# Kernel optimization log

Measured on AMD Instinct MI355X. Metric: run time of the kernel, lower is better.

## Reference

```python
import jax, jax.numpy as jnp
import numpy as np

B, S, D = 4, 4096, 1024
C = 8.0

def setup_inputs() -> dict:
    key = jax.random.key(0)
    k_x, k_wa, k_wx, k_ba, k_bx, k_lam = jax.random.split(key, 6)
    x = jax.random.normal(k_x, (B, S, D), dtype=jnp.float32)
    std = 1.0 / np.sqrt(D)
    Wa = jax.random.normal(k_wa, (D, D), dtype=jnp.float32) * std
    Wx = jax.random.normal(k_wx, (D, D), dtype=jnp.float32) * std
    ba = jax.random.normal(k_ba, (D,), dtype=jnp.float32) * 0.02
    bx = jax.random.normal(k_bx, (D,), dtype=jnp.float32) * 0.02
    # Lambda init: u ~ U(0.9, 0.999); Lambda = -log(u^{-1/c} - 1)
    u = jax.random.uniform(k_lam, (D,), dtype=jnp.float32, minval=0.9, maxval=0.999)
    Lam = -jnp.log(jnp.power(u, -1.0 / C) - 1.0)
    return {"x": x, "Wa": Wa, "Wx": Wx, "ba": ba, "bx": bx, "Lam": Lam}

def reference(x, Wa, Wx, ba, bx, Lam):
    # gates for all timesteps at once (two GEMMs)
    rt = jax.nn.sigmoid(jnp.einsum('bsd,hd->bsh', x, Wa) + ba)   # recurrence gate
    it = jax.nn.sigmoid(jnp.einsum('bsd,hd->bsh', x, Wx) + bx)   # input gate
    log_a = -C * jax.nn.softplus(-Lam) * rt                      # (B,S,D)
    a = jnp.exp(log_a)
    b = jnp.sqrt(1.0 - a * a) * (it * x)                         # (B,S,D)
    # sequential diagonal linear recurrence h_t = a_t * h_{t-1} + b_t
    def step(h, ab):
        a_t, b_t = ab
        h = a_t * h + b_t
        return h, h
    h0 = jnp.zeros((x.shape[0], x.shape[2]), dtype=x.dtype)
    _, y = jax.lax.scan(step, h0, (jnp.swapaxes(a, 0, 1), jnp.swapaxes(b, 0, 1)))
    return jnp.swapaxes(y, 0, 1)  # (B,S,D)
```

## Files before the change

### kernel.cpp

```cpp
#include <hip/hip_runtime.h>
#include <hip/hip_bf16.h>
#include <math.h>

#define BDIM 4
#define SLEN 4096
#define DDIM 1024
#define MROWS (BDIM*SLEN)
#define KDIM DDIM
#define NCHUNK 64
#define CLEN (SLEN/NCHUNK)
#define NCH (BDIM*DDIM)
#define NKT (KDIM/32)
#define LDSBUF 16384

typedef __bf16 bf16;
typedef __bf16 bf16x8 __attribute__((ext_vector_type(8)));
typedef float f32x16 __attribute__((ext_vector_type(16)));

__device__ __forceinline__ void gload_lds16(const void* g, void* l) {
  __builtin_amdgcn_global_load_lds(
      (const __attribute__((address_space(1))) unsigned int*)g,
      (__attribute__((address_space(3))) unsigned int*)l, 16, 0, 0);
}

__global__ void cast_swz_kernel(const float* __restrict__ in, bf16* __restrict__ out) {
  const int gid  = blockIdx.x * 256 + threadIdx.x;
  const int tile = gid >> 7, local = gid & 127;
  const int j = local & 3, r = local >> 2;
  const int T = tile >> 5, KT = tile & 31;
  const float4* src = (const float4*)(in + (size_t)(T*32 + r) * KDIM + KT*32 + j*8);
  float4 v0 = src[0], v1 = src[1];
  bf16x8 o;
  o[0] = (bf16)v0.x; o[1] = (bf16)v0.y; o[2] = (bf16)v0.z; o[3] = (bf16)v0.w;
  o[4] = (bf16)v1.x; o[5] = (bf16)v1.y; o[6] = (bf16)v1.z; o[7] = (bf16)v1.w;
  ((bf16x8*)out)[(size_t)tile * 128 + j*32 + r] = o;
}

__global__ void klam_kernel(const float* __restrict__ Lam, float* __restrict__ klam) {
  int h = blockIdx.x * blockDim.x + threadIdx.x;
  if (h < DDIM) klam[h] = -8.0f * log1pf(__expf(-Lam[h]));
}

__global__ __launch_bounds__(256, 3) void gemm_gates_kernel(
    const bf16* __restrict__ xb, const bf16* __restrict__ wab, const bf16* __restrict__ wxb,
    const float* __restrict__ ba, const float* __restrict__ bx,
    const float* __restrict__ klam, float* __restrict__ Aarr, bf16* __restrict__ Bp,
    float* __restrict__ sAo, float* __restrict__ sBo)
{
  __shared__ char smem[3*LDSBUF];

  const int tid  = threadIdx.x;
  const int wave = tid >> 6, lane = tid & 63;
  const int wm = wave >> 1, wn = wave & 1;

  const int orig  = blockIdx.x;
  const int newid = (orig & 7) * 256 + (orig >> 3);
  const int m0 = (newid >> 4) * 128;
  const int h0 = (newid & 15) * 64;

  f32x16 accA0 = (f32x16)0.0f, accA1 = (f32x16)0.0f;
  f32x16 accX0 = (f32x16)0.0f, accX1 = (f32x16)0.0f;

  const int Tb = m0 >> 5;
  const int Ht = h0 >> 5;
  const bf16* xsrc0 = xb  + (size_t)(Tb + (tid >> 7)) * 32768 + (tid & 127) * 8;
  const bf16* xsrc1 = xsrc0 + 2 * 32768;
  const bf16* wsrcA = wab + (size_t)(Ht + (tid >> 7)) * 32768 + (tid & 127) * 8;
  const bf16* wsrcX = wxb + (size_t)(Ht + (tid >> 7)) * 32768 + (tid & 127) * 8;

  auto STAGE = [&](int KT, char* nb) {
    gload_lds16(xsrc0 + KT*1024, nb + tid*16);
    gload_lds16(xsrc1 + KT*1024, nb + 4096  + tid*16);
    gload_lds16(wsrcA + KT*1024, nb + 8192  + tid*16);
    gload_lds16(wsrcX + KT*1024, nb + 12288 + tid*16);
  };

  const int awoff  = wm*4096  + lane*16;
  const int bwoffA = 8192  + wn*2048 + lane*16;
  const int bwoffX = 12288 + wn*2048 + lane*16;

  char* b0 = smem;
  char* b1 = smem + LDSBUF;
  char* b2 = smem + 2*LDSBUF;

  STAGE(0, b0);
  STAGE(1, b1);
  asm volatile("s_waitcnt vmcnt(4)" ::: "memory");
  __builtin_amdgcn_s_barrier();

  char *pc = b0, *pn = b1, *ps = b2;
  for (int kt = 0; kt < NKT; ++kt) {
    bf16x8 a00 = *(const bf16x8*)(pc + awoff);
    bf16x8 a01 = *(const bf16x8*)(pc + awoff + 1024);
    bf16x8 a10 = *(const bf16x8*)(pc + awoff + 2048);
    bf16x8 a11 = *(const bf16x8*)(pc + awoff + 3072);
    bf16x8 ba0 = *(const bf16x8*)(pc + bwoffA);
    bf16x8 ba1 = *(const bf16x8*)(pc + bwoffA + 1024);
    bf16x8 bx0 = *(const bf16x8*)(pc + bwoffX);
    bf16x8 bx1 = *(const bf16x8*)(pc + bwoffX + 1024);
    __builtin_amdgcn_sched_barrier(0);

    if (kt + 2 < NKT) STAGE(kt + 2, ps);

    __builtin_amdgcn_s_barrier();
    asm volatile("s_waitcnt lgkmcnt(0)" ::: "memory");
    __builtin_amdgcn_sched_barrier(0);

    __builtin_amdgcn_s_setprio(1);
    accA0 = __builtin_amdgcn_mfma_f32_32x32x16_bf16(a00, ba0, accA0, 0, 0, 0);
    accA1 = __builtin_amdgcn_mfma_f32_32x32x16_bf16(a10, ba0, accA1, 0, 0, 0);
    accX0 = __builtin_amdgcn_mfma_f32_32x32x16_bf16(a00, bx0, accX0, 0, 0, 0);
    accX1 = __builtin_amdgcn_mfma_f32_32x32x16_bf16(a10, bx0, accX1, 0, 0, 0);
    accA0 = __builtin_amdgcn_mfma_f32_32x32x16_bf16(a01, ba1, accA0, 0, 0, 0);
    accA1 = __builtin_amdgcn_mfma_f32_32x32x16_bf16(a11, ba1, accA1, 0, 0, 0);
    accX0 = __builtin_amdgcn_mfma_f32_32x32x16_bf16(a01, bx1, accX0, 0, 0, 0);
    accX1 = __builtin_amdgcn_mfma_f32_32x32x16_bf16(a11, bx1, accX1, 0, 0, 0);
    __builtin_amdgcn_s_setprio(0);

    if (kt + 2 < NKT)      { asm volatile("s_waitcnt vmcnt(4)" ::: "memory"); }
    else if (kt + 1 < NKT) { asm volatile("s_waitcnt vmcnt(0)" ::: "memory"); }
    if (kt + 1 < NKT) __builtin_amdgcn_s_barrier();

    char* tmp = pc; pc = pn; pn = ps; ps = tmp;
  }

  const int colh = h0 + wn*32 + (lane & 31);
  const int hi   = lane >> 5;
  const float bah = ba[colh], bxh = bx[colh], kl = klam[colh];
  const size_t xh = (size_t)(colh >> 5) * 1024 + ((colh >> 3) & 3) * 256 + (colh & 7);

  float P[2][4], S[2][4];
  #pragma unroll
  for (int mt = 0; mt < 2; ++mt) {
    const int mbase = m0 + wm*64 + mt*32;
    const size_t xtb = (size_t)(mbase >> 5) * 32768 + xh;
    const f32x16 aA = mt ? accA1 : accA0;
    const f32x16 aX = mt ? accX1 : accX0;
    #pragma unroll
    for (int g = 0; g < 4; ++g) {
      float Pg = 1.0f, Sg = 0.0f;
      #pragma unroll
      for (int jj = 0; jj < 4; ++jj) {
        const int q   = g*4 + jj;
        const int row = jj + 8*g + 4*hi;
        const int m   = mbase + row;
        const float ga = aA[q] + bah;
        const float gx = aX[q] + bxh;
        const float rt = 1.0f / (1.0f + __expf(-ga));
        const float it = 1.0f / (1.0f + __expf(-gx));
        const float a  = __expf(kl * rt);
        const float xv = (float)xb[xtb + (size_t)row * 8];
        const float bb = sqrtf(fmaxf(1.0f - a*a, 0.0f)) * (it * xv);
        Aarr[(size_t)m * DDIM + colh] = a;
        Bp[(size_t)m * DDIM + colh]   = (bf16)bb;
        Sg = fmaf(a, Sg, bb);
        Pg *= a;
      }
      P[mt][g] = Pg; S[mt][g] = Sg;
    }
  }

  float Pc = 1.0f, Sc = 0.0f;
  #pragma unroll
  for (int mt = 0; mt < 2; ++mt) {
    #pragma unroll
    for (int g = 0; g < 4; ++g) {
      const float pm = P[mt][g], sm = S[mt][g];
      const float pp = __shfl_xor(pm, 32);
      const float sp = __shfl_xor(sm, 32);
      const float p0 = hi ? pp : pm, s0 = hi ? sp : sm;
      const float p1 = hi ? pm : pp, s1 = hi ? sm : sp;
      Sc = fmaf(p0, Sc, s0); Pc *= p0;
      Sc = fmaf(p1, Sc, s1); Pc *= p1;
    }
  }
  if (hi == 0) {
    const int mb0  = m0 + wm*64;
    const int bidx = mb0 >> 12;
    const int c    = (mb0 & (SLEN-1)) >> 6;
    sAo[(size_t)c * NCH + bidx*1024 + colh] = Pc;
    sBo[(size_t)c * NCH + bidx*1024 + colh] = Sc;
  }
}

__global__ void scan2_kernel(const float* __restrict__ sA, const float* __restrict__ sB,
                             float* __restrict__ Hin) {
  const int ch = blockIdx.x * 256 + threadIdx.x;
  float h = 0.0f;
  for (int c = 0; c < NCHUNK; ++c) {
    Hin[c * NCH + ch] = h;
    h = fmaf(sA[c * NCH + ch], h, sB[c * NCH + ch]);
  }
}

__global__ void scan3_kernel(const bf16* __restrict__ Bp, const float* __restrict__ Hin,
                             float* __restrict__ y) {
  const int ch = blockIdx.x * 256 + threadIdx.x;
  const int c  = blockIdx.y;
  const int b  = ch >> 10, d = ch & 1023;
  size_t idx = ((size_t)b * SLEN + (size_t)c * CLEN) * DDIM + d;
  float h = Hin[c * NCH + ch];
  #pragma unroll 4
  for (int s = 0; s < CLEN; ++s) {
    const float a = y[idx];
    h = fmaf(a, h, (float)Bp[idx]);
    y[idx] = h;
    idx += DDIM;
  }
}

extern "C" void kernel_launch(void* const* d_in, const int* in_sizes, int n_in,
                              void* d_out, int out_size, void* d_ws, size_t ws_size,
                              hipStream_t stream) {
  const float* x   = (const float*)d_in[0];
  const float* Wa  = (const float*)d_in[1];
  const float* Wx  = (const float*)d_in[2];
  const float* ba  = (const float*)d_in[3];
  const float* bx  = (const float*)d_in[4];
  const float* Lam = (const float*)d_in[5];
  float* y = (float*)d_out;

  if (ws_size < 74452992ULL) return;
  char* ws = (char*)d_ws;
  bf16*  xb   = (bf16*)(ws);
  bf16*  wab  = (bf16*)(ws + 33554432);
  bf16*  wxb  = (bf16*)(ws + 35651584);
  bf16*  Bp   = (bf16*)(ws + 37748736);
  float* klam = (float*)(ws + 71303168);
  float* sA   = (float*)(ws + 71307264);
  float* sB   = (float*)(ws + 72355840);
  float* Hin  = (float*)(ws + 73404416);
  float* Aarr = y;

  cast_swz_kernel<<<(MROWS/32)*(KDIM/32)*128/256, 256, 0, stream>>>(x,  xb);
  cast_swz_kernel<<<(DDIM/32)*(KDIM/32)*128/256, 256, 0, stream>>>(Wa, wab);
  cast_swz_kernel<<<(DDIM/32)*(KDIM/32)*128/256, 256, 0, stream>>>(Wx, wxb);
  klam_kernel<<<DDIM/256, 256, 0, stream>>>(Lam, klam);

  gemm_gates_kernel<<<2048, 256, 0, stream>>>(xb, wab, wxb, ba, bx, klam,
                                              Aarr, Bp, sA, sB);

  scan2_kernel<<<NCH/256, 256, 0, stream>>>(sA, sB, Hin);
  dim3 sgrid(NCH/256, NCHUNK);
  scan3_kernel<<<sgrid, 256, 0, stream>>>(Bp, Hin, y);
}
```

Baseline: 149.0 us.

## Enlarge gate GEMM tile to 256x128 with 8 waves and 4-stage pipeline

Moves the fused gate GEMM from a 128x64 tile on 4 waves to a 256x128 tile on 8 waves (512 threads, 512 blocks). The pipeline becomes a 4-buffer prefetch three K-steps ahead, with the A and B loads split across two half-steps. The larger tile is meant to cut global and LDS traffic per MFMA, and the deeper prefetch is meant to hide load latency. In exchange it uses 128KB of LDS per block, needs more accumulator registers, and leaves fewer blocks to balance across CUs.

After: 151.3 us. About the same (+1.5%).

```diff
diff --git a/kernel.cpp b/kernel.cpp
--- a/kernel.cpp
+++ b/kernel.cpp
@@ -11,7 +11,7 @@
 #define CLEN (SLEN/NCHUNK)
 #define NCH (BDIM*DDIM)
 #define NKT (KDIM/32)
-#define LDSBUF 16384
+#define KBUF 32768
 
 typedef __bf16 bf16;
 typedef __bf16 bf16x8 __attribute__((ext_vector_type(8)));
@@ -41,87 +41,111 @@
   if (h < DDIM) klam[h] = -8.0f * log1pf(__expf(-Lam[h]));
 }
 
-__global__ __launch_bounds__(256, 3) void gemm_gates_kernel(
+#define MFMA32(A,B,C) C = __builtin_amdgcn_mfma_f32_32x32x16_bf16(A, B, C, 0, 0, 0)
+
+__global__ __launch_bounds__(512, 2) void gemm_gates_kernel(
     const bf16* __restrict__ xb, const bf16* __restrict__ wab, const bf16* __restrict__ wxb,
     const float* __restrict__ ba, const float* __restrict__ bx,
     const float* __restrict__ klam, float* __restrict__ Aarr, bf16* __restrict__ Bp,
     float* __restrict__ sAo, float* __restrict__ sBo)
 {
-  __shared__ char smem[3*LDSBUF];
+  __shared__ char smem[4*KBUF];
 
   const int tid  = threadIdx.x;
   const int wave = tid >> 6, lane = tid & 63;
-  const int wm = wave >> 1, wn = wave & 1;
+  const int wm = wave >> 2, wn = wave & 3;
 
   const int orig  = blockIdx.x;
-  const int newid = (orig & 7) * 256 + (orig >> 3);
-  const int m0 = (newid >> 4) * 128;
-  const int h0 = (newid & 15) * 64;
-
-  f32x16 accA0 = (f32x16)0.0f, accA1 = (f32x16)0.0f;
-  f32x16 accX0 = (f32x16)0.0f, accX1 = (f32x16)0.0f;
-
+  const int newid = (orig & 7) * 64 + (orig >> 3);
+  const int m0 = (newid >> 3) * 256;
+  const int h0 = (newid & 7) * 128;
   const int Tb = m0 >> 5;
-  const int Ht = h0 >> 5;
-  const bf16* xsrc0 = xb  + (size_t)(Tb + (tid >> 7)) * 32768 + (tid & 127) * 8;
-  const bf16* xsrc1 = xsrc0 + 2 * 32768;
-  const bf16* wsrcA = wab + (size_t)(Ht + (tid >> 7)) * 32768 + (tid & 127) * 8;
-  const bf16* wsrcX = wxb + (size_t)(Ht + (tid >> 7)) * 32768 + (tid & 127) * 8;
-
-  auto STAGE = [&](int KT, char* nb) {
-    gload_lds16(xsrc0 + KT*1024, nb + tid*16);
-    gload_lds16(xsrc1 + KT*1024, nb + 4096  + tid*16);
-    gload_lds16(wsrcA + KT*1024, nb + 8192  + tid*16);
-    gload_lds16(wsrcX + KT*1024, nb + 12288 + tid*16);
+  const int Hb = h0 >> 5;
+
+  f32x16 acc[4][2];
+  #pragma unroll
+  for (int i = 0; i < 4; i++) { acc[i][0] = (f32x16)0.0f; acc[i][1] = (f32x16)0.0f; }
+
+  const int tIdx = tid >> 7;
+  const int g8   = (tid & 127) * 8;
+  const int l16  = (tid & 127) * 16;
+  const bf16* aS0 = xb  + (size_t)(Tb + tIdx)     * 32768 + g8;
+  const bf16* aS1 = xb  + (size_t)(Tb + 4 + tIdx) * 32768 + g8;
+  const bf16* bSa = wab + (size_t)(Hb + tIdx)     * 32768 + g8;
+  const bf16* bSx = wxb + (size_t)(Hb + tIdx)     * 32768 + g8;
+  const int dA0 = tIdx*2048 + l16;
+  const int dA1 = (4 + tIdx)*2048 + l16;
+  const int dBa = 16384 + tIdx*2048 + l16;
+  const int dBx = 16384 + (4 + tIdx)*2048 + l16;
+
+  auto SA = [&](int kt, char* b) {
+    gload_lds16(aS0 + kt*1024, b + dA0);
+    gload_lds16(aS1 + kt*1024, b + dA1);
   };
-
-  const int awoff  = wm*4096  + lane*16;
-  const int bwoffA = 8192  + wn*2048 + lane*16;
-  const int bwoffX = 12288 + wn*2048 + lane*16;
-
-  char* b0 = smem;
-  char* b1 = smem + LDSBUF;
-  char* b2 = smem + 2*LDSBUF;
-
-  STAGE(0, b0);
-  STAGE(1, b1);
-  asm volatile("s_waitcnt vmcnt(4)" ::: "memory");
+  auto SB = [&](int kt, char* b) {
+    gload_lds16(bSa + kt*1024, b + dBa);
+    gload_lds16(bSx + kt*1024, b + dBx);
+  };
+
+  const int aOff = wm*8192 + lane*16;
+  const int bOa  = 16384 + wn*2048 + lane*16;
+  const int bOx  = 16384 + (4 + wn)*2048 + lane*16;
+
+  char* p0 = smem;
+  char* p1 = smem + KBUF;
+  char* p2 = smem + 2*KBUF;
+  char* p3 = smem + 3*KBUF;
+
+  SA(0, p0); SB(0, p0);
+  SA(1, p1); SB(1, p1);
+  SA(2, p2); SB(2, p2);
+  asm volatile("s_waitcnt vmcnt(8)" ::: "memory");
   __builtin_amdgcn_s_barrier();
 
-  char *pc = b0, *pn = b1, *ps = b2;
-  for (int kt = 0; kt < NKT; ++kt) {
-    bf16x8 a00 = *(const bf16x8*)(pc + awoff);
-    bf16x8 a01 = *(const bf16x8*)(pc + awoff + 1024);
-    bf16x8 a10 = *(const bf16x8*)(pc + awoff + 2048);
-    bf16x8 a11 = *(const bf16x8*)(pc + awoff + 3072);
-    bf16x8 ba0 = *(const bf16x8*)(pc + bwoffA);
-    bf16x8 ba1 = *(const bf16x8*)(pc + bwoffA + 1024);
-    bf16x8 bx0 = *(const bf16x8*)(pc + bwoffX);
-    bf16x8 bx1 = *(const bf16x8*)(pc + bwoffX + 1024);
-    __builtin_amdgcn_sched_barrier(0);
-
-    if (kt + 2 < NKT) STAGE(kt + 2, ps);
-
+  for (int t = 0; t < NKT; ++t) {
+    const bool st = (t + 3 < NKT);
+    bf16x8 a0 = *(const bf16x8*)(p0 + aOff);
+    bf16x8 a1 = *(const bf16x8*)(p0 + aOff + 2048);
+    bf16x8 a2 = *(const bf16x8*)(p0 + aOff + 4096);
+    bf16x8 a3 = *(const bf16x8*)(p0 + aOff + 6144);
+    bf16x8 bA = *(const bf16x8*)(p0 + bOa);
+    bf16x8 bX = *(const bf16x8*)(p0 + bOx);
+    __builtin_amdgcn_sched_barrier(0);
+    if (st) SA(t + 3, p3);
     __builtin_amdgcn_s_barrier();
     asm volatile("s_waitcnt lgkmcnt(0)" ::: "memory");
     __builtin_amdgcn_sched_barrier(0);
-
     __builtin_amdgcn_s_setprio(1);
-    accA0 = __builtin_amdgcn_mfma_f32_32x32x16_bf16(a00, ba0, accA0, 0, 0, 0);
-    accA1 = __builtin_amdgcn_mfma_f32_32x32x16_bf16(a10, ba0, accA1, 0, 0, 0);
-    accX0 = __builtin_amdgcn_mfma_f32_32x32x16_bf16(a00, bx0, accX0, 0, 0, 0);
-    accX1 = __builtin_amdgcn_mfma_f32_32x32x16_bf16(a10, bx0, accX1, 0, 0, 0);
-    accA0 = __builtin_amdgcn_mfma_f32_32x32x16_bf16(a01, ba1, accA0, 0, 0, 0);
-    accA1 = __builtin_amdgcn_mfma_f32_32x32x16_bf16(a11, ba1, accA1, 0, 0, 0);
-    accX0 = __builtin_amdgcn_mfma_f32_32x32x16_bf16(a01, bx1, accX0, 0, 0, 0);
-    accX1 = __builtin_amdgcn_mfma_f32_32x32x16_bf16(a11, bx1, accX1, 0, 0, 0);
+    MFMA32(a0, bA, acc[0][0]); MFMA32(a0, bX, acc[0][1]);
+    MFMA32(a1, bA, acc[1][0]); MFMA32(a1, bX, acc[1][1]);
+    MFMA32(a2, bA, acc[2][0]); MFMA32(a2, bX, acc[2][1]);
+    MFMA32(a3, bA, acc[3][0]); MFMA32(a3, bX, acc[3][1]);
     __builtin_amdgcn_s_setprio(0);
-
-    if (kt + 2 < NKT)      { asm volatile("s_waitcnt vmcnt(4)" ::: "memory"); }
-    else if (kt + 1 < NKT) { asm volatile("s_waitcnt vmcnt(0)" ::: "memory"); }
-    if (kt + 1 < NKT) __builtin_amdgcn_s_barrier();
-
-    char* tmp = pc; pc = pn; pn = ps; ps = tmp;
+    __builtin_amdgcn_s_barrier();
+
+    a0 = *(const bf16x8*)(p0 + aOff + 1024);
+    a1 = *(const bf16x8*)(p0 + aOff + 3072);
+    a2 = *(const bf16x8*)(p0 + aOff + 5120);
+    a3 = *(const bf16x8*)(p0 + aOff + 7168);
+    bA = *(const bf16x8*)(p0 + bOa + 1024);
+    bX = *(const bf16x8*)(p0 + bOx + 1024);
+    __builtin_amdgcn_sched_barrier(0);
+    if (st) SB(t + 3, p3);
+    if (t < NKT - 3)       { asm volatile("s_waitcnt vmcnt(8)" ::: "memory"); }
+    else if (t == NKT - 3) { asm volatile("s_waitcnt vmcnt(4)" ::: "memory"); }
+    else                   { asm volatile("s_waitcnt vmcnt(0)" ::: "memory"); }
+    __builtin_amdgcn_s_barrier();
+    asm volatile("s_waitcnt lgkmcnt(0)" ::: "memory");
+    __builtin_amdgcn_sched_barrier(0);
+    __builtin_amdgcn_s_setprio(1);
+    MFMA32(a0, bA, acc[0][0]); MFMA32(a0, bX, acc[0][1]);
+    MFMA32(a1, bA, acc[1][0]); MFMA32(a1, bX, acc[1][1]);
+    MFMA32(a2, bA, acc[2][0]); MFMA32(a2, bX, acc[2][1]);
+    MFMA32(a3, bA, acc[3][0]); MFMA32(a3, bX, acc[3][1]);
+    __builtin_amdgcn_s_setprio(0);
+    __builtin_amdgcn_s_barrier();
+
+    char* tp = p0; p0 = p1; p1 = p2; p2 = p3; p3 = tp;
   }
 
   const int colh = h0 + wn*32 + (lane & 31);
@@ -129,57 +153,58 @@
   const float bah = ba[colh], bxh = bx[colh], kl = klam[colh];
   const size_t xh = (size_t)(colh >> 5) * 1024 + ((colh >> 3) & 3) * 256 + (colh & 7);
 
-  float P[2][4], S[2][4];
   #pragma unroll
-  for (int mt = 0; mt < 2; ++mt) {
-    const int mbase = m0 + wm*64 + mt*32;
-    const size_t xtb = (size_t)(mbase >> 5) * 32768 + xh;
-    const f32x16 aA = mt ? accA1 : accA0;
-    const f32x16 aX = mt ? accX1 : accX0;
+  for (int c2 = 0; c2 < 2; ++c2) {
+    float P[2][4], S[2][4];
     #pragma unroll
-    for (int g = 0; g < 4; ++g) {
-      float Pg = 1.0f, Sg = 0.0f;
+    for (int ml = 0; ml < 2; ++ml) {
+      const int mi    = c2*2 + ml;
+      const int mbase = m0 + wm*128 + mi*32;
+      const size_t xtb = (size_t)(mbase >> 5) * 32768 + xh;
       #pragma unroll
-      for (int jj = 0; jj < 4; ++jj) {
-        const int q   = g*4 + jj;
-        const int row = jj + 8*g + 4*hi;
-        const int m   = mbase + row;
-        const float ga = aA[q] + bah;
-        const float gx = aX[q] + bxh;
-        const float rt = 1.0f / (1.0f + __expf(-ga));
-        const float it = 1.0f / (1.0f + __expf(-gx));
-        const float a  = __expf(kl * rt);
-        const float xv = (float)xb[xtb + (size_t)row * 8];
-        const float bb = sqrtf(fmaxf(1.0f - a*a, 0.0f)) * (it * xv);
-        Aarr[(size_t)m * DDIM + colh] = a;
-        Bp[(size_t)m * DDIM + colh]   = (bf16)bb;
-        Sg = fmaf(a, Sg, bb);
-        Pg *= a;
+      for (int g = 0; g < 4; ++g) {
+        float Pg = 1.0f, Sg = 0.0f;
+        #pragma unroll
+        for (int jj = 0; jj < 4; ++jj) {
+          const int q   = g*4 + jj;
+          const int row = jj + 8*g + 4*hi;
+          const int m   = mbase + row;
+          const float ga = acc[mi][0][q] + bah;
+          const float gx = acc[mi][1][q] + bxh;
+          const float rt = 1.0f / (1.0f + __expf(-ga));
+          const float it = 1.0f / (1.0f + __expf(-gx));
+          const float a  = __expf(kl * rt);
+          const float xv = (float)xb[xtb + (size_t)row * 8];
+          const float bb = sqrtf(fmaxf(1.0f - a*a, 0.0f)) * (it * xv);
+          Aarr[(size_t)m * DDIM + colh] = a;
+          Bp[(size_t)m * DDIM + colh]   = (bf16)bb;
+          Sg = fmaf(a, Sg, bb);
+          Pg *= a;
+        }
+        P[ml][g] = Pg; S[ml][g] = Sg;
       }
-      P[mt][g] = Pg; S[mt][g] = Sg;
     }
-  }
-
-  float Pc = 1.0f, Sc = 0.0f;
-  #pragma unroll
-  for (int mt = 0; mt < 2; ++mt) {
+    float Pc = 1.0f, Sc = 0.0f;
     #pragma unroll
-    for (int g = 0; g < 4; ++g) {
-      const float pm = P[mt][g], sm = S[mt][g];
-      const float pp = __shfl_xor(pm, 32);
-      const float sp = __shfl_xor(sm, 32);
-      const float p0 = hi ? pp : pm, s0 = hi ? sp : sm;
-      const float p1 = hi ? pm : pp, s1 = hi ? sm : sp;
-      Sc = fmaf(p0, Sc, s0); Pc *= p0;
-      Sc = fmaf(p1, Sc, s1); Pc *= p1;
+    for (int ml = 0; ml < 2; ++ml) {
+      #pragma unroll
+      for (int g = 0; g < 4; ++g) {
+        const float pm = P[ml][g], sm = S[ml][g];
+        const float pp = __shfl_xor(pm, 32);
+        const float sp = __shfl_xor(sm, 32);
+        const float p0v = hi ? pp : pm, s0v = hi ? sp : sm;
+        const float p1v = hi ? pm : pp, s1v = hi ? sm : sp;
+        Sc = fmaf(p0v, Sc, s0v); Pc *= p0v;
+        Sc = fmaf(p1v, Sc, s1v); Pc *= p1v;
+      }
     }
-  }
-  if (hi == 0) {
-    const int mb0  = m0 + wm*64;
-    const int bidx = mb0 >> 12;
-    const int c    = (mb0 & (SLEN-1)) >> 6;
-    sAo[(size_t)c * NCH + bidx*1024 + colh] = Pc;
-    sBo[(size_t)c * NCH + bidx*1024 + colh] = Sc;
+    if (hi == 0) {
+      const int mb0  = m0 + wm*128 + c2*64;
+      const int bidx = mb0 >> 12;
+      const int c    = (mb0 & (SLEN-1)) >> 6;
+      sAo[(size_t)c * NCH + bidx*1024 + colh] = Pc;
+      sBo[(size_t)c * NCH + bidx*1024 + colh] = Sc;
+    }
   }
 }
 
@@ -237,8 +262,8 @@
   cast_swz_kernel<<<(DDIM/32)*(KDIM/32)*128/256, 256, 0, stream>>>(Wx, wxb);
   klam_kernel<<<DDIM/256, 256, 0, stream>>>(Lam, klam);
 
-  gemm_gates_kernel<<<2048, 256, 0, stream>>>(xb, wab, wxb, ba, bx, klam,
-                                              Aarr, Bp, sA, sB);
+  gemm_gates_kernel<<<512, 512, 0, stream>>>(xb, wab, wxb, ba, bx, klam,
+                                             Aarr, Bp, sA, sB);
 
   scan2_kernel<<<NCH/256, 256, 0, stream>>>(sA, sB, Hin);
   dim3 sgrid(NCH/256, NCHUNK);
```

## Store log2 decay as bf16 instead of fp32 a, merge cast kernels

Applied to the files above, without the earlier changes.

The GEMM epilogue now writes the log2-domain decay as bf16 into a workspace buffer instead of writing fp32 a into the output. The scan kernel recomputes a with exp2, which halves the bytes written and read for that intermediate. The three cast launches are merged into one kernel over x, Wa and Wx, relying on the contiguous workspace layout. Quantizing log_a to bf16 adds relative error to a and to the recurrence, and the state shared across chunks still uses the fp32 a, so the two stages can disagree slightly.

Result: faster. 140.9 us (-5.4%).

```diff
diff --git a/kernel.cpp b/kernel.cpp
--- a/kernel.cpp
+++ b/kernel.cpp
@@ -12,6 +12,7 @@
 #define NCH (BDIM*DDIM)
 #define NKT (KDIM/32)
 #define LDSBUF 16384
+#define ALLROWS (MROWS + 2*DDIM)
 
 typedef __bf16 bf16;
 typedef __bf16 bf16x8 __attribute__((ext_vector_type(8)));
@@ -23,13 +24,20 @@
       (__attribute__((address_space(3))) unsigned int*)l, 16, 0, 0);
 }
 
-__global__ void cast_swz_kernel(const float* __restrict__ in, bf16* __restrict__ out) {
+__global__ void cast_all_kernel(const float* __restrict__ x, const float* __restrict__ Wa,
+                                const float* __restrict__ Wx, bf16* __restrict__ out) {
   const int gid  = blockIdx.x * 256 + threadIdx.x;
   const int tile = gid >> 7, local = gid & 127;
   const int j = local & 3, r = local >> 2;
   const int T = tile >> 5, KT = tile & 31;
-  const float4* src = (const float4*)(in + (size_t)(T*32 + r) * KDIM + KT*32 + j*8);
-  float4 v0 = src[0], v1 = src[1];
+  const int m = T*32 + r;
+  const float* src;
+  int row;
+  if (m < MROWS)              { src = x;  row = m; }
+  else if (m < MROWS + DDIM)  { src = Wa; row = m - MROWS; }
+  else                        { src = Wx; row = m - MROWS - DDIM; }
+  const float4* p = (const float4*)(src + (size_t)row * KDIM + KT*32 + j*8);
+  float4 v0 = p[0], v1 = p[1];
   bf16x8 o;
   o[0] = (bf16)v0.x; o[1] = (bf16)v0.y; o[2] = (bf16)v0.z; o[3] = (bf16)v0.w;
   o[4] = (bf16)v1.x; o[5] = (bf16)v1.y; o[6] = (bf16)v1.z; o[7] = (bf16)v1.w;
@@ -38,13 +46,13 @@
 
 __global__ void klam_kernel(const float* __restrict__ Lam, float* __restrict__ klam) {
   int h = blockIdx.x * blockDim.x + threadIdx.x;
-  if (h < DDIM) klam[h] = -8.0f * log1pf(__expf(-Lam[h]));
+  if (h < DDIM) klam[h] = -8.0f * 1.4426950408889634f * log1pf(__expf(-Lam[h]));
 }
 
 __global__ __launch_bounds__(256, 3) void gemm_gates_kernel(
     const bf16* __restrict__ xb, const bf16* __restrict__ wab, const bf16* __restrict__ wxb,
     const float* __restrict__ ba, const float* __restrict__ bx,
-    const float* __restrict__ klam, float* __restrict__ Aarr, bf16* __restrict__ Bp,
+    const float* __restrict__ klam, bf16* __restrict__ La, bf16* __restrict__ Bp,
     float* __restrict__ sAo, float* __restrict__ sBo)
 {
   __shared__ char smem[3*LDSBUF];
@@ -148,11 +156,12 @@
         const float gx = aX[q] + bxh;
         const float rt = 1.0f / (1.0f + __expf(-ga));
         const float it = 1.0f / (1.0f + __expf(-gx));
-        const float a  = __expf(kl * rt);
+        const float la = kl * rt;
+        const float a  = exp2f(la);
         const float xv = (float)xb[xtb + (size_t)row * 8];
         const float bb = sqrtf(fmaxf(1.0f - a*a, 0.0f)) * (it * xv);
-        Aarr[(size_t)m * DDIM + colh] = a;
-        Bp[(size_t)m * DDIM + colh]   = (bf16)bb;
+        La[(size_t)m * DDIM + colh] = (bf16)la;
+        Bp[(size_t)m * DDIM + colh] = (bf16)bb;
         Sg = fmaf(a, Sg, bb);
         Pg *= a;
       }
@@ -193,8 +202,8 @@
   }
 }
 
-__global__ void scan3_kernel(const bf16* __restrict__ Bp, const float* __restrict__ Hin,
-                             float* __restrict__ y) {
+__global__ void scan3_kernel(const bf16* __restrict__ La, const bf16* __restrict__ Bp,
+                             const float* __restrict__ Hin, float* __restrict__ y) {
   const int ch = blockIdx.x * 256 + threadIdx.x;
   const int c  = blockIdx.y;
   const int b  = ch >> 10, d = ch & 1023;
@@ -202,7 +211,7 @@
   float h = Hin[c * NCH + ch];
   #pragma unroll 4
   for (int s = 0; s < CLEN; ++s) {
-    const float a = y[idx];
+    const float a = exp2f((float)La[idx]);
     h = fmaf(a, h, (float)Bp[idx]);
     y[idx] = h;
     idx += DDIM;
@@ -220,27 +229,25 @@
   const float* Lam = (const float*)d_in[5];
   float* y = (float*)d_out;
 
-  if (ws_size < 74452992ULL) return;
+  if (ws_size < 108007424ULL) return;
   char* ws = (char*)d_ws;
   bf16*  xb   = (bf16*)(ws);
   bf16*  wab  = (bf16*)(ws + 33554432);
   bf16*  wxb  = (bf16*)(ws + 35651584);
   bf16*  Bp   = (bf16*)(ws + 37748736);
-  float* klam = (float*)(ws + 71303168);
-  float* sA   = (float*)(ws + 71307264);
-  float* sB   = (float*)(ws + 72355840);
-  float* Hin  = (float*)(ws + 73404416);
-  float* Aarr = y;
-
-  cast_swz_kernel<<<(MROWS/32)*(KDIM/32)*128/256, 256, 0, stream>>>(x,  xb);
-  cast_swz_kernel<<<(DDIM/32)*(KDIM/32)*128/256, 256, 0, stream>>>(Wa, wab);
-  cast_swz_kernel<<<(DDIM/32)*(KDIM/32)*128/256, 256, 0, stream>>>(Wx, wxb);
+  bf16*  La   = (bf16*)(ws + 71303168);
+  float* klam = (float*)(ws + 104857600);
+  float* sA   = (float*)(ws + 104861696);
+  float* sB   = (float*)(ws + 105910272);
+  float* Hin  = (float*)(ws + 106958848);
+
+  cast_all_kernel<<<(ALLROWS/32)*(KDIM/32)*128/256, 256, 0, stream>>>(x, Wa, Wx, xb);
   klam_kernel<<<DDIM/256, 256, 0, stream>>>(Lam, klam);
 
   gemm_gates_kernel<<<2048, 256, 0, stream>>>(xb, wab, wxb, ba, bx, klam,
-                                              Aarr, Bp, sA, sB);
+                                              La, Bp, sA, sB);
 
   scan2_kernel<<<NCH/256, 256, 0, stream>>>(sA, sB, Hin);
   dim3 sgrid(NCH/256, NCHUNK);
-  scan3_kernel<<<sgrid, 256, 0, stream>>>(Bp, Hin, y);
-}
+  scan3_kernel<<<sgrid, 256, 0, stream>>>(La, Bp, Hin, y);
+}
```
